# Optimization experiments

Measured on AMD Instinct MI355X. Metric: run time of the kernel, lower is better.

Reference implementation:

```python
import jax, jax.numpy as jnp
import numpy as np

B, N, M = 2, 2048, 1024
C, CTX, H = 1024, 1024, 16
D = C // H
HID = int(C * 4.0)
EPS = 1e-6


def _ln(h):
    # LayerNorm32: fp32 layernorm, eps=1e-6, no affine params
    h32 = h.astype(jnp.float32)
    mu = jnp.mean(h32, axis=-1, keepdims=True)
    var = jnp.var(h32, axis=-1, keepdims=True)
    return ((h32 - mu) * jax.lax.rsqrt(var + EPS)).astype(h.dtype)


def _sdpa(q, k, v):
    # q: [B,Q,H,D], k/v: [B,K,H,D]
    scale = 1.0 / np.sqrt(D)
    s = jnp.einsum('bqhd,bkhd->bhqk', q, k) * scale
    p = jax.nn.softmax(s, axis=-1)
    return jnp.einsum('bhqk,bkhd->bqhd', p, v)


def _forward(x, context, Wqkv, bqkv, Wos, bos, Wq, bq, Wkv, bkv, Woc, boc, W1, b1, W2, b2):
    Bx, Nx, _ = x.shape
    Mx = context.shape[1]
    # --- self-attention (attn_mode='full') ---
    h = _ln(x)
    qkv = (h @ Wqkv + bqkv).reshape(Bx, Nx, 3, H, D)
    q, k, v = qkv[:, :, 0], qkv[:, :, 1], qkv[:, :, 2]
    a = _sdpa(q, k, v).reshape(Bx, Nx, C)
    x = x + (a @ Wos + bos)
    # --- cross-attention (always 'full') ---
    h = _ln(x)
    q = (h @ Wq + bq).reshape(Bx, Nx, H, D)
    kv = (context @ Wkv + bkv).reshape(Bx, Mx, 2, H, D)
    k, v = kv[:, :, 0], kv[:, :, 1]
    a = _sdpa(q, k, v).reshape(Bx, Nx, C)
    x = x + (a @ Woc + boc)
    # --- FFN with tanh-approx GELU ---
    h = _ln(x)
    x = x + (jax.nn.gelu(h @ W1 + b1, approximate=True) @ W2 + b2)
    return x


def setup_inputs() -> dict:
    key = jax.random.key(0)
    ks = jax.random.split(key, 12)
    rn = lambda k, shape: (jax.random.normal(k, shape, jnp.float32) * 0.02)
    return {
        'x': jax.random.normal(ks[0], (B, N, C), jnp.float32),
        'context': jax.random.normal(ks[1], (B, M, CTX), jnp.float32),
        'Wqkv': rn(ks[2], (C, 3 * C)), 'bqkv': jnp.zeros((3 * C,), jnp.float32),
        'Wos': rn(ks[3], (C, C)), 'bos': jnp.zeros((C,), jnp.float32),
        'Wq': rn(ks[4], (C, C)), 'bq': jnp.zeros((C,), jnp.float32),
        'Wkv': rn(ks[5], (CTX, 2 * C)), 'bkv': jnp.zeros((2 * C,), jnp.float32),
        'Woc': rn(ks[6], (C, C)), 'boc': jnp.zeros((C,), jnp.float32),
        'W1': rn(ks[7], (C, HID)), 'b1': jnp.zeros((HID,), jnp.float32),
        'W2': rn(ks[8], (HID, C)), 'b2': jnp.zeros((C,), jnp.float32),
    }


def reference(x, context, Wqkv, bqkv, Wos, bos, Wq, bq, Wkv, bkv, Woc, boc, W1, b1, W2, b2):
    return _forward(x, context, Wqkv, bqkv, Wos, bos, Wq, bq, Wkv, bkv, Woc, boc, W1, b1, W2, b2)
```

## Files before the change

kernel.cpp:

```cpp
#include <hip/hip_runtime.h>
#include <cstdint>

typedef unsigned short u16;
typedef short bf16x8 __attribute__((ext_vector_type(8)));
typedef unsigned short u16x8 __attribute__((ext_vector_type(8)));
typedef float f32x4 __attribute__((ext_vector_type(4)));

__device__ __forceinline__ u16 f2bf(float f) {
  union { float f; uint32_t u; } v; v.f = f;
  uint32_t r = (v.u + 0x7fffu + ((v.u >> 16) & 1u)) >> 16;
  return (u16)r;
}

__device__ __forceinline__ void gload_lds16(const u16* g, u16* l) {
  __builtin_amdgcn_global_load_lds(
      (const __attribute__((address_space(1))) void*)g,
      (__attribute__((address_space(3))) void*)l, 16, 0, 0);
}

__global__ __launch_bounds__(256) void ln_kernel(const float* __restrict__ x,
                                                 u16* __restrict__ h) {
  const int row = blockIdx.x;
  const int tid = threadIdx.x;
  const float4 v = *reinterpret_cast<const float4*>(x + (long)row * 1024 + tid * 4);
  float s  = v.x + v.y + v.z + v.w;
  float ss = v.x * v.x + v.y * v.y + v.z * v.z + v.w * v.w;
#pragma unroll
  for (int off = 32; off >= 1; off >>= 1) {
    s  += __shfl_xor(s, off, 64);
    ss += __shfl_xor(ss, off, 64);
  }
  __shared__ float red[8];
  const int wave = tid >> 6, lane = tid & 63;
  if (lane == 0) { red[wave] = s; red[4 + wave] = ss; }
  __syncthreads();
  s  = red[0] + red[1] + red[2] + red[3];
  ss = red[4] + red[5] + red[6] + red[7];
  const float mu   = s * (1.0f / 1024.0f);
  const float var  = ss * (1.0f / 1024.0f) - mu * mu;
  const float rstd = rsqrtf(var + 1e-6f);
  ushort4 o;
  o.x = f2bf((v.x - mu) * rstd);
  o.y = f2bf((v.y - mu) * rstd);
  o.z = f2bf((v.z - mu) * rstd);
  o.w = f2bf((v.w - mu) * rstd);
  *reinterpret_cast<ushort4*>(h + (long)row * 1024 + tid * 4) = o;
}

struct WEnt { const float* W; u16* Wt; int K, N, tEnd; };
struct WEnts { WEnt e[7]; int n; };

__global__ __launch_bounds__(256) void wconvert_all(WEnts args) {
  __shared__ u16 tile[64][72];
  int t = blockIdx.x;
  int i = 0, tStart = 0;
  while (i < args.n - 1 && t >= args.e[i].tEnd) { tStart = args.e[i].tEnd; i++; }
  const float* W = args.e[i].W;
  u16* Wt = args.e[i].Wt;
  const int K = args.e[i].K, N = args.e[i].N;
  const int rel = t - tStart;
  const int ntn = N >> 6;
  const int tn = rel % ntn, tk = rel / ntn;
  const int n0 = tn * 64, k0 = tk * 64;

  const int th = threadIdx.x;
  const int c4 = (th & 15) * 4;
  const int r  = th >> 4;
#pragma unroll
  for (int ii = 0; ii < 4; ii++) {
    const int row = ii * 16 + r;
    const float4 v = *reinterpret_cast<const float4*>(W + (long)(k0 + row) * N + n0 + c4);
    tile[c4 + 0][row] = f2bf(v.x);
    tile[c4 + 1][row] = f2bf(v.y);
    tile[c4 + 2][row] = f2bf(v.z);
    tile[c4 + 3][row] = f2bf(v.w);
  }
  __syncthreads();
  const int c8 = (th & 7) * 8;
  const int rn = th >> 3;
#pragma unroll
  for (int ii = 0; ii < 2; ii++) {
    const int row = ii * 32 + rn;
    *reinterpret_cast<u16x8*>(Wt + (long)(n0 + row) * K + k0 + c8) =
        *reinterpret_cast<const u16x8*>(&tile[row][c8]);
  }
}

__global__ __launch_bounds__(256) void f2bf_kernel(const float* __restrict__ in,
                                                   u16* __restrict__ out) {
  const long i = ((long)blockIdx.x * 256 + threadIdx.x) * 4;
  const float4 v = *reinterpret_cast<const float4*>(in + i);
  ushort4 o;
  o.x = f2bf(v.x); o.y = f2bf(v.y); o.z = f2bf(v.z); o.w = f2bf(v.w);
  *reinterpret_cast<ushort4*>(out + i) = o;
}

__global__ __launch_bounds__(256) void vtrans(const u16* __restrict__ V,
                                              u16* __restrict__ Vt,
                                              int vStride, long vBatch, int nk) {
  __shared__ u16 tile[64][72];
  const int t = threadIdx.x;
  const int b = blockIdx.z, h = blockIdx.y, n0 = blockIdx.x * 64;
  const u16* vp = V + (long)b * vBatch + h * 64;
  u16* op = Vt + (long)(b * 16 + h) * 64 * (long)nk + n0;
  const int ch = t & 7;
#pragma unroll
  for (int i = 0; i < 2; i++) {
    const int n = (t >> 3) + i * 32;
    const u16x8 v = *reinterpret_cast<const u16x8*>(vp + (long)(n0 + n) * vStride + ch * 8);
#pragma unroll
    for (int j = 0; j < 8; j++) tile[ch * 8 + j][n] = v[j];
  }
  __syncthreads();
#pragma unroll
  for (int i = 0; i < 2; i++) {
    const int d = (t >> 3) + i * 32;
    *reinterpret_cast<u16x8*>(op + (long)d * nk + ch * 8) =
        *reinterpret_cast<const u16x8*>(&tile[d][ch * 8]);
  }
}

template <int TN, int SX, bool OUT_BF16, bool GELU_ACT, bool RES>
__global__ __launch_bounds__(256, 2) void gemm_bt(
    const u16* __restrict__ A, const u16* __restrict__ Bt,
    const float* __restrict__ bias, const float* __restrict__ res,
    void* __restrict__ Cout, int Ndim, int Kdim, int lx, int ly) {
  constexpr int NFRAG = TN / 32;
  __shared__ u16 Al[128 * 32];
  __shared__ u16 Bl[TN * 32];
  const int j = blockIdx.x;
  const int c = j & 7, kk = j >> 3;
  const int cx = c % SX, cy = c / SX;
  const int bx = cx * lx + (kk % lx);
  const int by = cy * ly + (kk / lx);
  const int m0 = by * 128, n0 = bx * TN;

  const int tid  = threadIdx.x;
  const int lane = tid & 63, wave = tid >> 6;
  const int quad = lane >> 4, l15 = lane & 15;
  const int wr = wave >> 1, wc = wave & 1;

  f32x4 acc[4][NFRAG];
  const f32x4 vzero = {0.f, 0.f, 0.f, 0.f};
#pragma unroll
  for (int i = 0; i < 4; i++)
#pragma unroll
    for (int jj = 0; jj < NFRAG; jj++) acc[i][jj] = vzero;

  const long rowOff = (long)(lane >> 2) * Kdim + (lane & 3) * 8;
  const u16* gA = A  + (long)m0 * Kdim + rowOff;
  const u16* gB = Bt + (long)n0 * Kdim + rowOff;

  for (int k0 = 0; k0 < Kdim; k0 += 32) {
    __syncthreads();
    gload_lds16(gA + (long)(wave * 16) * Kdim + k0,       &Al[wave * 512]);
    gload_lds16(gA + (long)((wave + 4) * 16) * Kdim + k0, &Al[(wave + 4) * 512]);
    gload_lds16(gB + (long)(wave * 16) * Kdim + k0,       &Bl[wave * 512]);
    if constexpr (TN == 128)
      gload_lds16(gB + (long)((wave + 4) * 16) * Kdim + k0, &Bl[(wave + 4) * 512]);
    __syncthreads();

    bf16x8 af[4], bfr[NFRAG];
#pragma unroll
    for (int mt = 0; mt < 4; mt++)
      af[mt] = *reinterpret_cast<const bf16x8*>(&Al[(wr * 64 + mt * 16 + l15) * 32 + quad * 8]);
#pragma unroll
    for (int nt = 0; nt < NFRAG; nt++)
      bfr[nt] = *reinterpret_cast<const bf16x8*>(&Bl[(wc * NFRAG * 16 + nt * 16 + l15) * 32 + quad * 8]);
#pragma unroll
    for (int mt = 0; mt < 4; mt++)
#pragma unroll
      for (int nt = 0; nt < NFRAG; nt++)
        acc[mt][nt] = __builtin_amdgcn_mfma_f32_16x16x32_bf16(af[mt], bfr[nt], acc[mt][nt], 0, 0, 0);
  }

#pragma unroll
  for (int nt = 0; nt < NFRAG; nt++) {
    const int col = n0 + wc * NFRAG * 16 + nt * 16 + l15;
    const float bv = bias[col];
#pragma unroll
    for (int mt = 0; mt < 4; mt++) {
#pragma unroll
      for (int r = 0; r < 4; r++) {
        const int row = m0 + wr * 64 + mt * 16 + quad * 4 + r;
        float y = acc[mt][nt][r] + bv;
        if (GELU_ACT) {
          const float t = 0.7978845608028654f * (y + 0.044715f * y * y * y);
          y = 0.5f * y * (1.0f + tanhf(t));
        }
        if (RES) y += res[(long)row * Ndim + col];
        if (OUT_BF16)
          ((u16*)Cout)[(long)row * Ndim + col] = f2bf(y);
        else
          ((float*)Cout)[(long)row * Ndim + col] = y;
      }
    }
  }
}

__global__ __launch_bounds__(256, 2) void attn_kernel(
    const u16* __restrict__ Q, const u16* __restrict__ K, const u16* __restrict__ Vt,
    u16* __restrict__ O, int nk, int qStride, int kStride, int oStride,
    long qBatch, long kBatch, long oBatch) {
  __shared__ u16 Kt[64 * 64];
  __shared__ u16 Vl[64 * 64];
  __shared__ u16 Pl[4][32 * 64];

  const int tid = threadIdx.x;
  const int lane = tid & 63, wave = tid >> 6;
  const int quad = lane >> 4, l15 = lane & 15;
  const int b = blockIdx.z, hh = blockIdx.y, qt = blockIdx.x;

  const u16* qp = Q + (long)b * qBatch + hh * 64;
  const u16* kp = K + (long)b * kBatch + hh * 64;
  const u16* vp = Vt + (long)(b * 16 + hh) * 64 * (long)nk;

  bf16x8 qf[2][2];
  const int qrow = qt * 128 + wave * 32 + l15;
#pragma unroll
  for (int qg = 0; qg < 2; qg++) {
    qf[qg][0] = *reinterpret_cast<const bf16x8*>(qp + (long)(qrow + qg * 16) * qStride + quad * 8);
    qf[qg][1] = *reinterpret_cast<const bf16x8*>(qp + (long)(qrow + qg * 16) * qStride + 32 + quad * 8);
  }

  const int r8 = lane >> 3;
  const int gcol = ((lane & 7) ^ r8) * 8;
  const u16* kgA = kp + (long)(wave * 8 + r8) * kStride + gcol;
  const u16* kgB = kp + (long)((wave + 4) * 8 + r8) * kStride + gcol;
  const u16* vgA = vp + (long)(wave * 8 + r8) * nk + gcol;
  const u16* vgB = vp + (long)((wave + 4) * 8 + r8) * nk + gcol;

  const int cF = (quad ^ (l15 & 7)) * 8;

  const f32x4 vzero = {0.f, 0.f, 0.f, 0.f};
  f32x4 oAcc[2][4];
  float lSt[2] = {0.f, 0.f};
#pragma unroll
  for (int qg = 0; qg < 2; qg++)
#pragma unroll
    for (int i = 0; i < 4; i++) oAcc[qg][i] = vzero;

  const float SCL = 0.18033688f;
  const int nTiles = nk >> 6;
  const long kAdv = (long)64 * kStride;

  for (int kt = 0; kt < nTiles; kt++) {
    __syncthreads();
    gload_lds16(kgA + kt * kAdv, &Kt[wave * 512]);
    gload_lds16(kgB + kt * kAdv, &Kt[(wave + 4) * 512]);
    gload_lds16(vgA + kt * 64,   &Vl[wave * 512]);
    gload_lds16(vgB + kt * 64,   &Vl[(wave + 4) * 512]);
    __syncthreads();

    f32x4 st[2][4];
#pragma unroll
    for (int mt = 0; mt < 4; mt++) {
      const bf16x8 kf0 = *reinterpret_cast<const bf16x8*>(&Kt[(mt * 16 + l15) * 64 + cF]);
      const bf16x8 kf1 = *reinterpret_cast<const bf16x8*>(&Kt[(mt * 16 + l15) * 64 + (cF ^ 32)]);
#pragma unroll
      for (int qg = 0; qg < 2; qg++) {
        f32x4 z = vzero;
        z = __builtin_amdgcn_mfma_f32_16x16x32_bf16(kf0, qf[qg][0], z, 0, 0, 0);
        z = __builtin_amdgcn_mfma_f32_16x16x32_bf16(kf1, qf[qg][1], z, 0, 0, 0);
        st[qg][mt] = z;
      }
    }

#pragma unroll
    for (int qg = 0; qg < 2; qg++) {
      float ps = 0.f;
#pragma unroll
      for (int mt = 0; mt < 4; mt++)
#pragma unroll
        for (int r = 0; r < 4; r++) {
          const float p = __builtin_amdgcn_exp2f(st[qg][mt][r] * SCL);
          st[qg][mt][r] = p;
          ps += p;
        }
      lSt[qg] += ps;
      u16* plw = &Pl[wave][(qg * 16 + l15) * 64];
#pragma unroll
      for (int mt = 0; mt < 4; mt++) {
        union { float f; uint32_t u; } a0, a1, a2, a3;
        a0.f = st[qg][mt][0]; a1.f = st[qg][mt][1];
        a2.f = st[qg][mt][2]; a3.f = st[qg][mt][3];
        a0.u += 0x8000u; a1.u += 0x8000u; a2.u += 0x8000u; a3.u += 0x8000u;
        uint2 w;
        w.x = __builtin_amdgcn_perm(a1.u, a0.u, 0x07060302u);
        w.y = __builtin_amdgcn_perm(a3.u, a2.u, 0x07060302u);
        const int pcol = (((mt * 2 + (quad >> 1)) ^ (l15 & 7)) * 8) + (quad & 1) * 4;
        *reinterpret_cast<uint2*>(&plw[pcol]) = w;
      }
    }

    bf16x8 pf[2][2];
#pragma unroll
    for (int qg = 0; qg < 2; qg++) {
      const u16* plw = &Pl[wave][(qg * 16 + l15) * 64];
      pf[qg][0] = *reinterpret_cast<const bf16x8*>(&plw[cF]);
      pf[qg][1] = *reinterpret_cast<const bf16x8*>(&plw[cF ^ 32]);
    }
#pragma unroll
    for (int dt = 0; dt < 4; dt++) {
      const bf16x8 vf0 = *reinterpret_cast<const bf16x8*>(&Vl[(dt * 16 + l15) * 64 + cF]);
      const bf16x8 vf1 = *reinterpret_cast<const bf16x8*>(&Vl[(dt * 16 + l15) * 64 + (cF ^ 32)]);
#pragma unroll
      for (int qg = 0; qg < 2; qg++) {
        oAcc[qg][dt] = __builtin_amdgcn_mfma_f32_16x16x32_bf16(pf[qg][0], vf0, oAcc[qg][dt], 0, 0, 0);
        oAcc[qg][dt] = __builtin_amdgcn_mfma_f32_16x16x32_bf16(pf[qg][1], vf1, oAcc[qg][dt], 0, 0, 0);
      }
    }
  }

  u16* op = O + (long)b * oBatch + hh * 64;
#pragma unroll
  for (int qg = 0; qg < 2; qg++) {
    float l = lSt[qg];
    l += __shfl_xor(l, 16, 64);
    l += __shfl_xor(l, 32, 64);
    float lR[4];
#pragma unroll
    for (int r = 0; r < 4; r++) lR[r] = 1.0f / __shfl(l, quad * 4 + r, 64);
#pragma unroll
    for (int dt = 0; dt < 4; dt++)
#pragma unroll
      for (int r = 0; r < 4; r++) {
        const int row = qt * 128 + wave * 32 + qg * 16 + quad * 4 + r;
        op[(long)row * oStride + dt * 16 + l15] = f2bf(oAcc[qg][dt][r] * lR[r]);
      }
  }
}

extern "C" void kernel_launch(void* const* d_in, const int* in_sizes, int n_in,
                              void* d_out, int out_size, void* d_ws, size_t ws_size,
                              hipStream_t stream) {
  const float* x    = (const float*)d_in[0];
  const float* ctx  = (const float*)d_in[1];
  const float* Wqkv = (const float*)d_in[2];
  const float* bqkv = (const float*)d_in[3];
  const float* Wos  = (const float*)d_in[4];
  const float* bos  = (const float*)d_in[5];
  const float* Wq   = (const float*)d_in[6];
  const float* bq   = (const float*)d_in[7];
  const float* Wkv  = (const float*)d_in[8];
  const float* bkv  = (const float*)d_in[9];
  const float* Woc  = (const float*)d_in[10];
  const float* boc  = (const float*)d_in[11];
  const float* W1   = (const float*)d_in[12];
  const float* b1   = (const float*)d_in[13];
  const float* W2   = (const float*)d_in[14];
  const float* b2   = (const float*)d_in[15];
  float* out = (float*)d_out;
  char* ws = (char*)d_ws;
  const size_t MB = 1024 * 1024;

  if (ws_size >= 80 * MB) {
    u16* Wqkvt = (u16*)(ws + 0 * MB);
    u16* Wost  = (u16*)(ws + 6 * MB);
    u16* Wqt   = (u16*)(ws + 8 * MB);
    u16* Wkvt  = (u16*)(ws + 10 * MB);
    u16* Woct  = (u16*)(ws + 14 * MB);
    u16* W1t   = (u16*)(ws + 16 * MB);
    u16* W2t   = (u16*)(ws + 24 * MB);
    u16* h     = (u16*)(ws + 32 * MB);
    u16* abuf  = (u16*)(ws + 40 * MB);
    u16* qkv   = (u16*)(ws + 48 * MB);
    u16* q2    = (u16*)(ws + 48 * MB);
    u16* kv2   = (u16*)(ws + 56 * MB);
    u16* ctxbf = (u16*)(ws + 64 * MB);
    u16* VtCr  = (u16*)(ws + 68 * MB);
    u16* hid   = (u16*)(ws + 48 * MB);
    u16* VtSelf = h;

    WEnts we;
    we.n = 7;
    we.e[0] = {Wqkv, Wqkvt, 1024, 3072, 768};
    we.e[1] = {Wos,  Wost,  1024, 1024, 1024};
    we.e[2] = {Wq,   Wqt,   1024, 1024, 1280};
    we.e[3] = {Wkv,  Wkvt,  1024, 2048, 1792};
    we.e[4] = {Woc,  Woct,  1024, 1024, 2048};
    we.e[5] = {W1,   W1t,   1024, 4096, 3072};
    we.e[6] = {W2,   W2t,   4096, 1024, 4096};
    wconvert_all<<<dim3(4096), dim3(256), 0, stream>>>(we);
    f2bf_kernel<<<dim3(2048), dim3(256), 0, stream>>>(ctx, ctxbf);

    ln_kernel<<<dim3(4096), dim3(256), 0, stream>>>(x, h);
    gemm_bt<128, 2, true, false, false><<<dim3(768), dim3(256), 0, stream>>>(
        h, Wqkvt, bqkv, nullptr, qkv, 3072, 1024, 12, 8);
    vtrans<<<dim3(32, 16, 2), dim3(256), 0, stream>>>(
        qkv + 2048, VtSelf, 3072, (long)2048 * 3072, 2048);
    attn_kernel<<<dim3(16, 16, 2), dim3(256), 0, stream>>>(
        qkv, qkv + 1024, VtSelf, abuf, 2048, 3072, 3072, 1024,
        (long)2048 * 3072, (long)2048 * 3072, (long)2048 * 1024);
    gemm_bt<64, 1, false, false, true><<<dim3(512), dim3(256), 0, stream>>>(
        abuf, Wost, bos, x, out, 1024, 1024, 16, 4);
    ln_kernel<<<dim3(4096), dim3(256), 0, stream>>>(out, h);
    gemm_bt<64, 1, true, false, false><<<dim3(512), dim3(256), 0, stream>>>(
        h, Wqt, bq, nullptr, q2, 1024, 1024, 16, 4);
    gemm_bt<64, 2, true, false, false><<<dim3(512), dim3(256), 0, stream>>>(
        ctxbf, Wkvt, bkv, nullptr, kv2, 2048, 1024, 16, 4);
    vtrans<<<dim3(16, 16, 2), dim3(256), 0, stream>>>(
        kv2 + 1024, VtCr, 2048, (long)1024 * 2048, 1024);
    attn_kernel<<<dim3(16, 16, 2), dim3(256), 0, stream>>>(
        q2, kv2, VtCr, abuf, 1024, 1024, 2048, 1024,
        (long)2048 * 1024, (long)1024 * 2048, (long)2048 * 1024);
    gemm_bt<64, 1, false, false, true><<<dim3(512), dim3(256), 0, stream>>>(
        abuf, Woct, boc, out, out, 1024, 1024, 16, 4);
    ln_kernel<<<dim3(4096), dim3(256), 0, stream>>>(out, h);
    gemm_bt<128, 2, true, true, false><<<dim3(1024), dim3(256), 0, stream>>>(
        h, W1t, b1, nullptr, hid, 4096, 1024, 16, 8);
    gemm_bt<64, 2, false, false, true><<<dim3(512), dim3(256), 0, stream>>>(
        hid, W2t, b2, out, out, 1024, 4096, 8, 8);
  } else {
    u16* h      = (u16*)ws;
    u16* wbuf   = (u16*)(ws + 8 * MB);
    char* C0    = ws + 16 * MB;
    u16* qkv    = (u16*)C0;
    u16* Wqkvt  = (u16*)(C0 + 24 * MB);
    u16* Wost   = (u16*)C0;
    u16* q2     = (u16*)C0;
    u16* kv2    = (u16*)(C0 + 8 * MB);
    u16* Wqt    = (u16*)(C0 + 16 * MB);
    u16* Wkvt   = (u16*)(C0 + 16 * MB);
    u16* ctxbf  = (u16*)(C0 + 20 * MB);
    u16* VtCr   = (u16*)(C0 + 24 * MB);
    u16* Woct   = (u16*)(C0 + 16 * MB);
    u16* hid    = (u16*)C0;
    u16* VtSelf = h;
    u16* abuf   = wbuf;
    u16* W1t    = wbuf;
    u16* W2t    = wbuf;
    WEnts w1; w1.n = 1;

    ln_kernel<<<dim3(4096), dim3(256), 0, stream>>>(x, h);
    w1.e[0] = {Wqkv, Wqkvt, 1024, 3072, 768};
    wconvert_all<<<dim3(768), dim3(256), 0, stream>>>(w1);
    gemm_bt<128, 2, true, false, false><<<dim3(768), dim3(256), 0, stream>>>(
        h, Wqkvt, bqkv, nullptr, qkv, 3072, 1024, 12, 8);
    vtrans<<<dim3(32, 16, 2), dim3(256), 0, stream>>>(
        qkv + 2048, VtSelf, 3072, (long)2048 * 3072, 2048);
    attn_kernel<<<dim3(16, 16, 2), dim3(256), 0, stream>>>(
        qkv, qkv + 1024, VtSelf, abuf, 2048, 3072, 3072, 1024,
        (long)2048 * 3072, (long)2048 * 3072, (long)2048 * 1024);
    w1.e[0] = {Wos, Wost, 1024, 1024, 256};
    wconvert_all<<<dim3(256), dim3(256), 0, stream>>>(w1);
    gemm_bt<64, 1, false, false, true><<<dim3(512), dim3(256), 0, stream>>>(
        abuf, Wost, bos, x, out, 1024, 1024, 16, 4);
    ln_kernel<<<dim3(4096), dim3(256), 0, stream>>>(out, h);
    w1.e[0] = {Wq, Wqt, 1024, 1024, 256};
    wconvert_all<<<dim3(256), dim3(256), 0, stream>>>(w1);
    gemm_bt<64, 1, true, false, false><<<dim3(512), dim3(256), 0, stream>>>(
        h, Wqt, bq, nullptr, q2, 1024, 1024, 16, 4);
    f2bf_kernel<<<dim3(2048), dim3(256), 0, stream>>>(ctx, ctxbf);
    w1.e[0] = {Wkv, Wkvt, 1024, 2048, 512};
    wconvert_all<<<dim3(512), dim3(256), 0, stream>>>(w1);
    gemm_bt<64, 2, true, false, false><<<dim3(512), dim3(256), 0, stream>>>(
        ctxbf, Wkvt, bkv, nullptr, kv2, 2048, 1024, 16, 4);
    vtrans<<<dim3(16, 16, 2), dim3(256), 0, stream>>>(
        kv2 + 1024, VtCr, 2048, (long)1024 * 2048, 1024);
    attn_kernel<<<dim3(16, 16, 2), dim3(256), 0, stream>>>(
        q2, kv2, VtCr, abuf, 1024, 1024, 2048, 1024,
        (long)2048 * 1024, (long)1024 * 2048, (long)2048 * 1024);
    w1.e[0] = {Woc, Woct, 1024, 1024, 256};
    wconvert_all<<<dim3(256), dim3(256), 0, stream>>>(w1);
    gemm_bt<64, 1, false, false, true><<<dim3(512), dim3(256), 0, stream>>>(
        abuf, Woct, boc, out, out, 1024, 1024, 16, 4);
    ln_kernel<<<dim3(4096), dim3(256), 0, stream>>>(out, h);
    w1.e[0] = {W1, W1t, 1024, 4096, 1024};
    wconvert_all<<<dim3(1024), dim3(256), 0, stream>>>(w1);
    gemm_bt<128, 2, true, true, false><<<dim3(1024), dim3(256), 0, stream>>>(
        h, W1t, b1, nullptr, hid, 4096, 1024, 16, 8);
    w1.e[0] = {W2, W2t, 4096, 1024, 1024};
    wconvert_all<<<dim3(1024), dim3(256), 0, stream>>>(w1);
    gemm_bt<64, 2, false, false, true><<<dim3(512), dim3(256), 0, stream>>>(
        hid, W2t, b2, out, out, 1024, 4096, 8, 8);
  }
}
```

Baseline: 495.3 us.

## Double-buffer LDS tiles in GEMM and attention; widen W2 GEMM tile

Both the GEMM and attention kernels now keep two LDS buffers. The next K-tile is fetched with global_load_lds while the current tile is consumed, which removes one barrier per iteration and overlaps memory latency with MFMA work. The FFN down-projection GEMM also switches to 128-wide N tiles with half as many blocks. The cost is doubled LDS per block, which may limit occupancy. The larger W2 tile leaves fewer blocks to spread across CUs.

Result: no change. 486.0 us (-1.9%).

```diff
diff --git a/kernel.cpp b/kernel.cpp
--- a/kernel.cpp
+++ b/kernel.cpp
@@ -126,8 +126,8 @@
     const float* __restrict__ bias, const float* __restrict__ res,
     void* __restrict__ Cout, int Ndim, int Kdim, int lx, int ly) {
   constexpr int NFRAG = TN / 32;
-  __shared__ u16 Al[128 * 32];
-  __shared__ u16 Bl[TN * 32];
+  __shared__ u16 Al[2][128 * 32];
+  __shared__ u16 Bl[2][TN * 32];
   const int j = blockIdx.x;
   const int c = j & 7, kk = j >> 3;
   const int cx = c % SX, cy = c / SX;
@@ -151,22 +151,26 @@
   const u16* gA = A  + (long)m0 * Kdim + rowOff;
   const u16* gB = Bt + (long)n0 * Kdim + rowOff;
 
-  for (int k0 = 0; k0 < Kdim; k0 += 32) {
+  auto stage = [&](int k0, int p) {
+    gload_lds16(gA + (long)(wave * 16) * Kdim + k0,       &Al[p][wave * 512]);
+    gload_lds16(gA + (long)((wave + 4) * 16) * Kdim + k0, &Al[p][(wave + 4) * 512]);
+    gload_lds16(gB + (long)(wave * 16) * Kdim + k0,       &Bl[p][wave * 512]);
+    if constexpr (TN == 128)
+      gload_lds16(gB + (long)((wave + 4) * 16) * Kdim + k0, &Bl[p][(wave + 4) * 512]);
+  };
+
+  stage(0, 0);
+  int p = 0;
+  for (int k0 = 0; k0 < Kdim; k0 += 32, p ^= 1) {
     __syncthreads();
-    gload_lds16(gA + (long)(wave * 16) * Kdim + k0,       &Al[wave * 512]);
-    gload_lds16(gA + (long)((wave + 4) * 16) * Kdim + k0, &Al[(wave + 4) * 512]);
-    gload_lds16(gB + (long)(wave * 16) * Kdim + k0,       &Bl[wave * 512]);
-    if constexpr (TN == 128)
-      gload_lds16(gB + (long)((wave + 4) * 16) * Kdim + k0, &Bl[(wave + 4) * 512]);
-    __syncthreads();
-
     bf16x8 af[4], bfr[NFRAG];
 #pragma unroll
     for (int mt = 0; mt < 4; mt++)
-      af[mt] = *reinterpret_cast<const bf16x8*>(&Al[(wr * 64 + mt * 16 + l15) * 32 + quad * 8]);
+      af[mt] = *reinterpret_cast<const bf16x8*>(&Al[p][(wr * 64 + mt * 16 + l15) * 32 + quad * 8]);
 #pragma unroll
     for (int nt = 0; nt < NFRAG; nt++)
-      bfr[nt] = *reinterpret_cast<const bf16x8*>(&Bl[(wc * NFRAG * 16 + nt * 16 + l15) * 32 + quad * 8]);
+      bfr[nt] = *reinterpret_cast<const bf16x8*>(&Bl[p][(wc * NFRAG * 16 + nt * 16 + l15) * 32 + quad * 8]);
+    if (k0 + 32 < Kdim) stage(k0 + 32, p ^ 1);
 #pragma unroll
     for (int mt = 0; mt < 4; mt++)
 #pragma unroll
@@ -202,8 +206,8 @@
     const u16* __restrict__ Q, const u16* __restrict__ K, const u16* __restrict__ Vt,
     u16* __restrict__ O, int nk, int qStride, int kStride, int oStride,
     long qBatch, long kBatch, long oBatch) {
-  __shared__ u16 Kt[64 * 64];
-  __shared__ u16 Vl[64 * 64];
+  __shared__ u16 Kt[2][64 * 64];
+  __shared__ u16 Vl[2][64 * 64];
   __shared__ u16 Pl[4][32 * 64];
 
   const int tid = threadIdx.x;
@@ -244,19 +248,24 @@
   const int nTiles = nk >> 6;
   const long kAdv = (long)64 * kStride;
 
-  for (int kt = 0; kt < nTiles; kt++) {
+  auto stage = [&](int kt, int p) {
+    gload_lds16(kgA + kt * kAdv, &Kt[p][wave * 512]);
+    gload_lds16(kgB + kt * kAdv, &Kt[p][(wave + 4) * 512]);
+    gload_lds16(vgA + kt * 64,   &Vl[p][wave * 512]);
+    gload_lds16(vgB + kt * 64,   &Vl[p][(wave + 4) * 512]);
+  };
+
+  stage(0, 0);
+  int p = 0;
+  for (int kt = 0; kt < nTiles; kt++, p ^= 1) {
     __syncthreads();
-    gload_lds16(kgA + kt * kAdv, &Kt[wave * 512]);
-    gload_lds16(kgB + kt * kAdv, &Kt[(wave + 4) * 512]);
-    gload_lds16(vgA + kt * 64,   &Vl[wave * 512]);
-    gload_lds16(vgB + kt * 64,   &Vl[(wave + 4) * 512]);
-    __syncthreads();
+    if (kt + 1 < nTiles) stage(kt + 1, p ^ 1);
 
     f32x4 st[2][4];
 #pragma unroll
     for (int mt = 0; mt < 4; mt++) {
-      const bf16x8 kf0 = *reinterpret_cast<const bf16x8*>(&Kt[(mt * 16 + l15) * 64 + cF]);
-      const bf16x8 kf1 = *reinterpret_cast<const bf16x8*>(&Kt[(mt * 16 + l15) * 64 + (cF ^ 32)]);
+      const bf16x8 kf0 = *reinterpret_cast<const bf16x8*>(&Kt[p][(mt * 16 + l15) * 64 + cF]);
+      const bf16x8 kf1 = *reinterpret_cast<const bf16x8*>(&Kt[p][(mt * 16 + l15) * 64 + (cF ^ 32)]);
 #pragma unroll
       for (int qg = 0; qg < 2; qg++) {
         f32x4 z = vzero;
@@ -273,9 +282,9 @@
       for (int mt = 0; mt < 4; mt++)
 #pragma unroll
         for (int r = 0; r < 4; r++) {
-          const float p = __builtin_amdgcn_exp2f(st[qg][mt][r] * SCL);
-          st[qg][mt][r] = p;
-          ps += p;
+          const float pw = __builtin_amdgcn_exp2f(st[qg][mt][r] * SCL);
+          st[qg][mt][r] = pw;
+          ps += pw;
         }
       lSt[qg] += ps;
       u16* plw = &Pl[wave][(qg * 16 + l15) * 64];
@@ -302,8 +311,8 @@
     }
 #pragma unroll
     for (int dt = 0; dt < 4; dt++) {
-      const bf16x8 vf0 = *reinterpret_cast<const bf16x8*>(&Vl[(dt * 16 + l15) * 64 + cF]);
-      const bf16x8 vf1 = *reinterpret_cast<const bf16x8*>(&Vl[(dt * 16 + l15) * 64 + (cF ^ 32)]);
+      const bf16x8 vf0 = *reinterpret_cast<const bf16x8*>(&Vl[p][(dt * 16 + l15) * 64 + cF]);
+      const bf16x8 vf1 = *reinterpret_cast<const bf16x8*>(&Vl[p][(dt * 16 + l15) * 64 + (cF ^ 32)]);
 #pragma unroll
       for (int qg = 0; qg < 2; qg++) {
         oAcc[qg][dt] = __builtin_amdgcn_mfma_f32_16x16x32_bf16(pf[qg][0], vf0, oAcc[qg][dt], 0, 0, 0);
@@ -409,8 +418,8 @@
     ln_kernel<<<dim3(4096), dim3(256), 0, stream>>>(out, h);
     gemm_bt<128, 2, true, true, false><<<dim3(1024), dim3(256), 0, stream>>>(
         h, W1t, b1, nullptr, hid, 4096, 1024, 16, 8);
-    gemm_bt<64, 2, false, false, true><<<dim3(512), dim3(256), 0, stream>>>(
-        hid, W2t, b2, out, out, 1024, 4096, 8, 8);
+    gemm_bt<128, 2, false, false, true><<<dim3(256), dim3(256), 0, stream>>>(
+        hid, W2t, b2, out, out, 1024, 4096, 4, 8);
   } else {
     u16* h      = (u16*)ws;
     u16* wbuf   = (u16*)(ws + 8 * MB);
@@ -472,7 +481,7 @@
         h, W1t, b1, nullptr, hid, 4096, 1024, 16, 8);
     w1.e[0] = {W2, W2t, 4096, 1024, 1024};
     wconvert_all<<<dim3(1024), dim3(256), 0, stream>>>(w1);
-    gemm_bt<64, 2, false, false, true><<<dim3(512), dim3(256), 0, stream>>>(
-        hid, W2t, b2, out, out, 1024, 4096, 8, 8);
-  }
-}
+    gemm_bt<128, 2, false, false, true><<<dim3(256), dim3(256), 0, stream>>>(
+        hid, W2t, b2, out, out, 1024, 4096, 4, 8);
+  }
+}
```
